# Optimization experiments

Measured on AMD Instinct MI355X. Metric: run time of the kernel, lower is better.

## Reference

```python
import jax, jax.numpy as jnp
import numpy as np

HYP_C = 0.1
TAU = 0.1
MRG = 0.1
CLIP_R = 2.3
BS = 1024
NB_PROXIES = 256
SZ_EMBED = 128
T_BATCH = BS * 50
T_LCA = NB_PROXIES * 50


@jax.custom_vjp
def artanh(x):
    xc = jnp.clip(x, -1.0 + 1e-5, 1.0 - 1e-5)
    return 0.5 * (jnp.log1p(xc) - jnp.log1p(-xc))

def _artanh_fwd(x):
    xc = jnp.clip(x, -1.0 + 1e-5, 1.0 - 1e-5)
    return 0.5 * (jnp.log1p(xc) - jnp.log1p(-xc)), xc

def _artanh_bwd(xc, g):
    return (g / (1.0 - xc * xc),)

artanh.defvjp(_artanh_fwd, _artanh_bwd)


@jax.custom_vjp
def riemannian_fix(x):
    # identity fwd; bwd rescales euclidean grad to riemannian grad on the ball
    return x

def _riem_fwd(x):
    return x, x

def _riem_bwd(x, g):
    scale = ((1.0 - HYP_C * jnp.sum(x * x, axis=-1, keepdims=True)) ** 2) / 4.0
    return (g * scale,)

riemannian_fix.defvjp(_riem_fwd, _riem_bwd)


def expmap0(x, c):
    sqrt_c = c ** 0.5
    xn = jnp.maximum(jnp.linalg.norm(x, axis=-1, keepdims=True), 1e-5)
    return jnp.tanh(sqrt_c * xn) * x / (sqrt_c * xn)


def project(x, c):
    norm = jnp.maximum(jnp.linalg.norm(x, axis=-1, keepdims=True), 1e-5)
    maxnorm = (1.0 - 1e-3) / (c ** 0.5)
    return jnp.where(norm > maxnorm, x / norm * maxnorm, x)


def to_poincare(x, c, clip_r):
    xn = jnp.linalg.norm(x, axis=-1, keepdims=True) + 1e-5
    x = x * jnp.minimum(jnp.ones_like(xn), clip_r / xn)
    return riemannian_fix(project(expmap0(x, c), c))


def dist_matrix(x, y, c):
    # ||mobius_add(-x, y)|| computed in closed form (same math as the [N,M,D]
    # num/denom construction in the torch code; num_{nm} = a*( -x_n ) + b*y_m).
    sqrt_c = c ** 0.5
    xy = -jnp.einsum('nd,md->nm', x, y)        # (-x) . y
    x2 = jnp.sum(x * x, axis=-1, keepdims=True)  # [N,1]
    y2t = jnp.sum(y * y, axis=-1)[None, :]       # [1,M]
    a = 1.0 + 2.0 * c * xy + c * y2t             # coeff of -x
    b = 1.0 - c * x2                             # coeff of y
    denom = 1.0 + 2.0 * c * xy + (c ** 2) * x2 * y2t
    num_sq = a * a * x2 + 2.0 * a * b * xy + b * b * y2t
    norm = jnp.sqrt(jnp.maximum(num_sq, 1e-12)) / jnp.abs(denom + 1e-5)
    return (2.0 / sqrt_c) * artanh(sqrt_c * norm)


def gumbel_softmax_hard(logits, g):
    # straight-through hard gumbel softmax (tau=1 as in F.gumbel_softmax default)
    y = jax.nn.softmax(logits + g, axis=-1)
    hard = jax.nn.one_hot(jnp.argmax(y, axis=-1), y.shape[-1], dtype=y.dtype)
    return y + jax.lax.stop_gradient(hard - y)


def compute_ghhc(cp_dist, trip, g):
    i, j, k = trip[0], trip[1], trip[2]
    di, dj, dk = cp_dist[i], cp_dist[j], cp_dist[k]   # [T,P] each
    max_ij = jnp.maximum(di, dj)
    p_ij = gumbel_softmax_hard(-max_ij / TAU, g[0])
    max_ijk = jnp.maximum(dk, max_ij)
    p_ijk = gumbel_softmax_hard(-max_ijk / TAU, g[1])
    diff_lca = (jnp.argmax(p_ij, -1) != jnp.argmax(p_ijk, -1)).astype(cp_dist.dtype)
    d_i_ij = jnp.sum(di * p_ij, axis=1)
    d_i_ijk = jnp.sum(di * p_ijk, axis=1)
    d_j_ij = jnp.sum(dj * p_ij, axis=1)
    d_j_ijk = jnp.sum(dj * p_ijk, axis=1)
    d_k_ij = jnp.sum(dk * p_ij, axis=1)
    d_k_ijk = jnp.sum(dk * p_ijk, axis=1)
    hc = (jax.nn.relu(d_i_ij - d_i_ijk + MRG)
          + jax.nn.relu(d_j_ij - d_j_ijk + MRG)
          + jax.nn.relu(d_k_ijk - d_k_ij + MRG))
    return jnp.mean(hc * diff_lca)


def hp_loss(z_s, t_s, lcas, trip1, trip2, trip3, trip4, g1, g2, g3, g4):
    bs = z_s.shape[0]
    lh = to_poincare(lcas, HYP_C, CLIP_R)
    all_nodes = jnp.concatenate([z_s, lh], axis=0)
    D = dist_matrix(all_nodes, all_nodes, HYP_C)
    t_all = jnp.concatenate([t_s, lh], axis=0)
    Dt = dist_matrix(t_all, t_all, HYP_C)
    loss = compute_ghhc(D[:bs, bs:], trip1, g1)
    loss = loss + compute_ghhc(D[bs:, bs:], trip2, g2)
    loss = loss + compute_ghhc(Dt[:bs, bs:], trip3, g3)
    loss = loss + compute_ghhc(Dt[bs:, bs:], trip4, g4)
    return loss


def setup_inputs() -> dict:
    key = jax.random.key(0)
    ks = jax.random.split(key, 12)
    z_s = jax.random.normal(ks[0], (BS, SZ_EMBED), dtype=jnp.float32)
    t_s = jax.random.normal(ks[1], (BS, SZ_EMBED), dtype=jnp.float32)
    y = jax.random.uniform(ks[2], (BS, 24), dtype=jnp.float32)
    # lcas param init: randn / sqrt(d) * clip_r * 0.9
    lcas = jax.random.normal(ks[3], (NB_PROXIES, SZ_EMBED), dtype=jnp.float32)
    lcas = lcas / np.sqrt(SZ_EMBED) * CLIP_R * 0.9
    trip1 = jax.random.randint(ks[4], (3, T_BATCH), 0, BS, dtype=jnp.int32)
    trip2 = jax.random.randint(ks[5], (3, T_LCA), 0, NB_PROXIES, dtype=jnp.int32)
    trip3 = jax.random.randint(ks[6], (3, T_BATCH), 0, BS, dtype=jnp.int32)
    trip4 = jax.random.randint(ks[7], (3, T_LCA), 0, NB_PROXIES, dtype=jnp.int32)
    g1 = jax.random.gumbel(ks[8], (2, T_BATCH, NB_PROXIES), dtype=jnp.float32)
    g2 = jax.random.gumbel(ks[9], (2, T_LCA, NB_PROXIES), dtype=jnp.float32)
    g3 = jax.random.gumbel(ks[10], (2, T_BATCH, NB_PROXIES), dtype=jnp.float32)
    g4 = jax.random.gumbel(ks[11], (2, T_LCA, NB_PROXIES), dtype=jnp.float32)
    return {"z_s": z_s, "t_s": t_s, "y": y, "lcas": lcas,
            "trip1": trip1, "trip2": trip2, "trip3": trip3, "trip4": trip4,
            "g1": g1, "g2": g2, "g3": g3, "g4": g4}


def reference(z_s, t_s, y, lcas, trip1, trip2, trip3, trip4, g1, g2, g3, g4):
    # y only feeds the detached numpy mining loop in the original; the mined
    # triplets are supplied precomputed (trip1..4), so y does not enter the math.
    return hp_loss(z_s, t_s, lcas, trip1, trip2, trip3, trip4, g1, g2, g3, g4)
```

## Files before the change

### kernel.cpp

```cpp
#include <hip/hip_runtime.h>
#include <cstddef>
#include <stdint.h>

#define HYP_C   0.1f
#define SQRT_C  0.31622776601683794f
#define CLIP_R  2.3f
#define MRG     0.1f
#define NPROX   256
#define DIM     128

#define OFF_LH   0
#define OFF_LHT  32768
#define OFF_LN2  65536
#define OFF_D1   65792
#define OFF_D2   327936
#define OFF_D3   393472

__global__ __launch_bounds__(128)
void to_poincare_kernel(const float* __restrict__ lcas,
                        float* __restrict__ ws,
                        float* __restrict__ out)
{
    const int row = blockIdx.x;
    const int k   = threadIdx.x;
    if (row == 0 && k == 0) out[0] = 0.0f;

    float v  = lcas[row * DIM + k];
    float ss = v * v;
    #pragma unroll
    for (int off = 32; off >= 1; off >>= 1)
        ss += __shfl_xor(ss, off, 64);
    __shared__ float wpart[2];
    if ((k & 63) == 0) wpart[k >> 6] = ss;
    __syncthreads();
    const float sumsq = wpart[0] + wpart[1];

    const float s1 = sqrtf(sumsq);
    const float xn = s1 + 1e-5f;
    const float f1 = fminf(1.0f, CLIP_R / xn);
    const float xn2 = fmaxf(f1 * s1, 1e-5f);
    const float th  = tanhf(SQRT_C * xn2);
    const float f2  = th / (SQRT_C * xn2);
    const float nr      = fmaxf(f2 * f1 * s1, 1e-5f);
    const float maxnorm = (1.0f - 1e-3f) / SQRT_C;
    const float f3      = (nr > maxnorm) ? (maxnorm / nr) : 1.0f;

    const float f  = f3 * f2 * f1;
    const float lv = f * v;
    ws[OFF_LH  + row * DIM + k]   = lv;
    ws[OFF_LHT + k * NPROX + row] = lv;
    if (k == 0) ws[OFF_LN2 + row] = f * f * sumsq;
}

__global__ __launch_bounds__(256)
void dist_all_kernel(const float* __restrict__ z,
                     const float* __restrict__ t,
                     float* __restrict__ ws, int nb1)
{
    const float* lhT = ws + OFF_LHT;
    const float* ln2 = ws + OFF_LN2;

    int b = blockIdx.x;
    const float* X; float* Dout; int row0;
    if (b < nb1)            { X = z;            Dout = ws + OFF_D1; row0 = b * 4; }
    else if (b < nb1 + 64)  { X = ws + OFF_LH;  Dout = ws + OFF_D2; row0 = (b - nb1) * 4; }
    else                    { X = t;            Dout = ws + OFF_D3; row0 = (b - nb1 - 64) * 4; }

    __shared__ float xs[4][DIM];
    __shared__ float sx2[4];

    for (int idx = threadIdx.x; idx < 4 * DIM; idx += 256)
        xs[idx / DIM][idx % DIM] = X[row0 * DIM + idx];
    __syncthreads();

    const int wid  = threadIdx.x >> 6;
    const int lane = threadIdx.x & 63;
    {
        float a = xs[wid][lane];
        float c = xs[wid][lane + 64];
        float s = a * a + c * c;
        #pragma unroll
        for (int off = 32; off >= 1; off >>= 1)
            s += __shfl_xor(s, off, 64);
        if (lane == 0) sx2[wid] = s;
    }
    __syncthreads();

    const int m = threadIdx.x;
    float dot0 = 0.f, dot1 = 0.f, dot2 = 0.f, dot3 = 0.f;
    #pragma unroll 8
    for (int k = 0; k < DIM; k += 4) {
        const float4 x0 = *(const float4*)&xs[0][k];
        const float4 x1 = *(const float4*)&xs[1][k];
        const float4 x2 = *(const float4*)&xs[2][k];
        const float4 x3 = *(const float4*)&xs[3][k];
        const float l0 = lhT[(k + 0) * NPROX + m];
        const float l1 = lhT[(k + 1) * NPROX + m];
        const float l2 = lhT[(k + 2) * NPROX + m];
        const float l3 = lhT[(k + 3) * NPROX + m];
        dot0 = fmaf(x0.x, l0, fmaf(x0.y, l1, fmaf(x0.z, l2, fmaf(x0.w, l3, dot0))));
        dot1 = fmaf(x1.x, l0, fmaf(x1.y, l1, fmaf(x1.z, l2, fmaf(x1.w, l3, dot1))));
        dot2 = fmaf(x2.x, l0, fmaf(x2.y, l1, fmaf(x2.z, l2, fmaf(x2.w, l3, dot2))));
        dot3 = fmaf(x3.x, l0, fmaf(x3.y, l1, fmaf(x3.z, l2, fmaf(x3.w, l3, dot3))));
    }

    const float y2 = ln2[m];
    float dots[4] = {dot0, dot1, dot2, dot3};
    #pragma unroll
    for (int r = 0; r < 4; ++r) {
        const float x2 = sx2[r];
        const float xy = -dots[r];
        const float a  = 1.0f + 2.0f * HYP_C * xy + HYP_C * y2;
        const float bb = 1.0f - HYP_C * x2;
        const float denom  = 1.0f + 2.0f * HYP_C * xy + HYP_C * HYP_C * x2 * y2;
        const float num_sq = a * a * x2 + 2.0f * a * bb * xy + bb * bb * y2;
        const float nrm = sqrtf(fmaxf(num_sq, 1e-12f)) / fabsf(denom + 1e-5f);
        float u = SQRT_C * nrm;
        u = fminf(fmaxf(u, -1.0f + 1e-5f), 1.0f - 1e-5f);
        const float d = (2.0f / SQRT_C) * (0.5f * (log1pf(u) - log1pf(-u)));
        Dout[(size_t)(row0 + r) * NPROX + m] = d;
    }
}

__device__ __forceinline__ float dpp_fmax16(float x) {
    int o;
    o = __builtin_amdgcn_update_dpp(0, __float_as_int(x), 0x121, 0xF, 0xF, true);
    x = fmaxf(x, __int_as_float(o));
    o = __builtin_amdgcn_update_dpp(0, __float_as_int(x), 0x122, 0xF, 0xF, true);
    x = fmaxf(x, __int_as_float(o));
    o = __builtin_amdgcn_update_dpp(0, __float_as_int(x), 0x124, 0xF, 0xF, true);
    x = fmaxf(x, __int_as_float(o));
    o = __builtin_amdgcn_update_dpp(0, __float_as_int(x), 0x128, 0xF, 0xF, true);
    x = fmaxf(x, __int_as_float(o));
    return x;
}

__device__ __forceinline__ int dpp_imax16(int x) {
    int o;
    o = __builtin_amdgcn_update_dpp(0, x, 0x121, 0xF, 0xF, true); x = max(x, o);
    o = __builtin_amdgcn_update_dpp(0, x, 0x122, 0xF, 0xF, true); x = max(x, o);
    o = __builtin_amdgcn_update_dpp(0, x, 0x124, 0xF, 0xF, true); x = max(x, o);
    o = __builtin_amdgcn_update_dpp(0, x, 0x128, 0xF, 0xF, true); x = max(x, o);
    return x;
}

__device__ __forceinline__ void amax4(float v0, float v1, float v2, float v3,
                                      int base, float& lv, int& li)
{
    if (v0 > lv) { lv = v0; li = base; }
    if (v1 > lv) { lv = v1; li = base + 1; }
    if (v2 > lv) { lv = v2; li = base + 2; }
    if (v3 > lv) { lv = v3; li = base + 3; }
}

__global__ __launch_bounds__(64, 4)
void ghhc_fused_kernel(const float* __restrict__ Da, const float* __restrict__ Db,
                       const float* __restrict__ Dc, const float* __restrict__ Dd,
                       const int* __restrict__ ta, const int* __restrict__ tb,
                       const int* __restrict__ tc, const int* __restrict__ td,
                       const float* __restrict__ ga, const float* __restrict__ gb,
                       const float* __restrict__ gc, const float* __restrict__ gd,
                       int Ta, int Tb, int Tc, int Td,
                       float sa, float sb, float sc_, float sd,
                       int nba, int nbb, int nbc,
                       float* __restrict__ out)
{
    const int lane = threadIdx.x;
    const int grp  = lane >> 4;
    const int hl   = lane & 15;

    const int b = blockIdx.x;
    const float* D; const int* tr; const float* g; int Tt; float sc; int lb;
    if (b < nba)                   { D = Da; tr = ta; g = ga; Tt = Ta; sc = sa;  lb = b; }
    else if (b < nba + nbb)        { D = Db; tr = tb; g = gb; Tt = Tb; sc = sb;  lb = b - nba; }
    else if (b < nba + nbb + nbc)  { D = Dc; tr = tc; g = gc; Tt = Tc; sc = sc_; lb = b - nba - nbb; }
    else                           { D = Dd; tr = td; g = gd; Tt = Td; sc = sd;  lb = b - nba - nbb - nbc; }

    const int tstart = lb * 32;
    float acc = 0.0f;

    #pragma unroll 2
    for (int it = 0; it < 8; ++it) {
        const int tt = tstart + it * 4 + grp;
        const bool ok = tt < Tt;
        const int ts = ok ? tt : (Tt - 1);
        const int i = tr[ts], j = tr[Tt + ts], kk = tr[2 * Tt + ts];

        const float4* Di = (const float4*)(D + (size_t)i  * NPROX);
        const float4* Dj = (const float4*)(D + (size_t)j  * NPROX);
        const float4* Dk = (const float4*)(D + (size_t)kk * NPROX);
        const float4* G0 = (const float4*)(g + (size_t)ts * NPROX);
        const float4* G1 = (const float4*)(g + ((size_t)Tt + ts) * NPROX);

        float lvA = -__builtin_inff(), lvB = -__builtin_inff();
        int   liA = 0, liB = 0;

        #pragma unroll
        for (int m = 0; m < 4; ++m) {
            const int q = m * 16 + hl;
            const float4 di = Di[q], dj = Dj[q], dk = Dk[q];
            const float4 g0 = G0[q], g1 = G1[q];

            const float m1x = fmaxf(di.x, dj.x), m1y = fmaxf(di.y, dj.y),
                        m1z = fmaxf(di.z, dj.z), m1w = fmaxf(di.w, dj.w);
            const float sx = fmaf(m1x, -10.0f, g0.x), sy = fmaf(m1y, -10.0f, g0.y),
                        sz = fmaf(m1z, -10.0f, g0.z), sw = fmaf(m1w, -10.0f, g0.w);
            const float m2x = fmaxf(dk.x, m1x), m2y = fmaxf(dk.y, m1y),
                        m2z = fmaxf(dk.z, m1z), m2w = fmaxf(dk.w, m1w);
            const float ux = fmaf(m2x, -10.0f, g1.x), uy = fmaf(m2y, -10.0f, g1.y),
                        uz = fmaf(m2z, -10.0f, g1.z), uw = fmaf(m2w, -10.0f, g1.w);

            const int base = m * 64 + hl * 4;
            amax4(sx, sy, sz, sw, base, lvA, liA);
            amax4(ux, uy, uz, uw, base, lvB, liB);
        }

        const float gvA = dpp_fmax16(lvA);
        const int   A   = 255 - dpp_imax16((lvA == gvA) ? (255 - liA) : 0);
        const float gvB = dpp_fmax16(lvB);
        const int   B   = 255 - dpp_imax16((lvB == gvB) ? (255 - liB) : 0);

        const float diA = D[(size_t)i  * NPROX + A], diB = D[(size_t)i  * NPROX + B];
        const float djA = D[(size_t)j  * NPROX + A], djB = D[(size_t)j  * NPROX + B];
        const float dkA = D[(size_t)kk * NPROX + A], dkB = D[(size_t)kk * NPROX + B];
        const float hc = fmaxf(diA - diB + MRG, 0.0f)
                       + fmaxf(djA - djB + MRG, 0.0f)
                       + fmaxf(dkB - dkA + MRG, 0.0f);
        acc += (ok && (A != B) && (hl == 0)) ? hc * sc : 0.0f;
    }

    #pragma unroll
    for (int off = 32; off >= 1; off >>= 1)
        acc += __shfl_xor(acc, off, 64);
    if (lane == 0)
        atomicAdd(out, acc);
}

extern "C" void kernel_launch(void* const* d_in, const int* in_sizes, int n_in,
                              void* d_out, int out_size, void* d_ws, size_t ws_size,
                              hipStream_t stream)
{
    const float* z_s  = (const float*)d_in[0];
    const float* t_s  = (const float*)d_in[1];
    const float* lcas = (const float*)d_in[3];
    const int* trip1 = (const int*)d_in[4];
    const int* trip2 = (const int*)d_in[5];
    const int* trip3 = (const int*)d_in[6];
    const int* trip4 = (const int*)d_in[7];
    const float* g1 = (const float*)d_in[8];
    const float* g2 = (const float*)d_in[9];
    const float* g3 = (const float*)d_in[10];
    const float* g4 = (const float*)d_in[11];
    float* out = (float*)d_out;
    float* ws  = (float*)d_ws;

    const int T1 = in_sizes[4] / 3;
    const int T2 = in_sizes[5] / 3;
    const int T3 = in_sizes[6] / 3;
    const int T4 = in_sizes[7] / 3;
    const int BS = in_sizes[0] / DIM;
    const int nb1 = BS / 4;

    to_poincare_kernel<<<NPROX, 128, 0, stream>>>(lcas, ws, out);

    dist_all_kernel<<<2 * nb1 + 64, 256, 0, stream>>>(z_s, t_s, ws, nb1);

    const int nbA = (T1 + 31) / 32;
    const int nbB = (T2 + 31) / 32;
    const int nbC = (T3 + 31) / 32;
    const int nbD = (T4 + 31) / 32;
    ghhc_fused_kernel<<<nbA + nbB + nbC + nbD, 64, 0, stream>>>(
        ws + OFF_D1, ws + OFF_D2, ws + OFF_D3, ws + OFF_D2,
        trip1, trip2, trip3, trip4,
        g1, g2, g3, g4,
        T1, T2, T3, T4,
        1.0f / (float)T1, 1.0f / (float)T2, 1.0f / (float)T3, 1.0f / (float)T4,
        nbA, nbB, nbC,
        out);
}
```

Baseline: 350.9 us.

## Restructure triplet argmax kernel: register-held rows, DPP value broadcast, 256-thread blocks

Each wave now handles 16 triplets per block, and blocks grow from 64 to 256 threads. Triplet indices are prefetched up front. The D and Gumbel rows are held in registers, so the argmax winner's distances are broadcast with DPP max reductions instead of being re-gathered with six scattered global loads. Argmax tie-breaking now keeps the lowest index through a separate pass plus a DPP min. The cross-wave sum goes through shared memory, so there are fewer atomics. The aim is to cut dependent global gathers and per-block overhead, at the cost of more register pressure and less per-wave triplet work.

```diff
diff --git a/kernel.cpp b/kernel.cpp
--- a/kernel.cpp
+++ b/kernel.cpp
@@ -135,25 +135,16 @@
     return x;
 }
 
-__device__ __forceinline__ int dpp_imax16(int x) {
+__device__ __forceinline__ int dpp_imin16(int x) {
     int o;
-    o = __builtin_amdgcn_update_dpp(0, x, 0x121, 0xF, 0xF, true); x = max(x, o);
-    o = __builtin_amdgcn_update_dpp(0, x, 0x122, 0xF, 0xF, true); x = max(x, o);
-    o = __builtin_amdgcn_update_dpp(0, x, 0x124, 0xF, 0xF, true); x = max(x, o);
-    o = __builtin_amdgcn_update_dpp(0, x, 0x128, 0xF, 0xF, true); x = max(x, o);
+    o = __builtin_amdgcn_update_dpp(0, x, 0x121, 0xF, 0xF, true); x = min(x, o);
+    o = __builtin_amdgcn_update_dpp(0, x, 0x122, 0xF, 0xF, true); x = min(x, o);
+    o = __builtin_amdgcn_update_dpp(0, x, 0x124, 0xF, 0xF, true); x = min(x, o);
+    o = __builtin_amdgcn_update_dpp(0, x, 0x128, 0xF, 0xF, true); x = min(x, o);
     return x;
 }
 
-__device__ __forceinline__ void amax4(float v0, float v1, float v2, float v3,
-                                      int base, float& lv, int& li)
-{
-    if (v0 > lv) { lv = v0; li = base; }
-    if (v1 > lv) { lv = v1; li = base + 1; }
-    if (v2 > lv) { lv = v2; li = base + 2; }
-    if (v3 > lv) { lv = v3; li = base + 3; }
-}
-
-__global__ __launch_bounds__(64, 4)
+__global__ __launch_bounds__(256)
 void ghhc_fused_kernel(const float* __restrict__ Da, const float* __restrict__ Db,
                        const float* __restrict__ Dc, const float* __restrict__ Dd,
                        const int* __restrict__ ta, const int* __restrict__ tb,
@@ -165,9 +156,11 @@
                        int nba, int nbb, int nbc,
                        float* __restrict__ out)
 {
-    const int lane = threadIdx.x;
-    const int grp  = lane >> 4;
-    const int hl   = lane & 15;
+    const int tid = threadIdx.x;
+    const int w   = tid >> 6;
+    const int grp = (tid >> 4) & 3;
+    const int hl  = tid & 15;
+    const int hl4 = hl << 2;
 
     const int b = blockIdx.x;
     const float* D; const int* tr; const float* g; int Tt; float sc; int lb;
@@ -176,64 +169,98 @@
     else if (b < nba + nbb + nbc)  { D = Dc; tr = tc; g = gc; Tt = Tc; sc = sc_; lb = b - nba - nbb; }
     else                           { D = Dd; tr = td; g = gd; Tt = Td; sc = sd;  lb = b - nba - nbb - nbc; }
 
-    const int tstart = lb * 32;
+    const int tstart = lb * 64 + w * 16;
+
+    int iIt[4], jIt[4], kIt[4]; bool okIt[4];
+    #pragma unroll
+    for (int it = 0; it < 4; ++it) {
+        int t = tstart + it * 4 + grp;
+        okIt[it] = (t < Tt);
+        t = okIt[it] ? t : (Tt - 1);
+        iIt[it] = tr[t]; jIt[it] = tr[Tt + t]; kIt[it] = tr[2 * Tt + t];
+    }
+
     float acc = 0.0f;
 
-    #pragma unroll 2
-    for (int it = 0; it < 8; ++it) {
-        const int tt = tstart + it * 4 + grp;
-        const bool ok = tt < Tt;
-        const int ts = ok ? tt : (Tt - 1);
-        const int i = tr[ts], j = tr[Tt + ts], kk = tr[2 * Tt + ts];
+    #pragma unroll 1
+    for (int it = 0; it < 4; ++it) {
+        int t = tstart + it * 4 + grp;
+        t = okIt[it] ? t : (Tt - 1);
+        const int i = iIt[it], j = jIt[it], kk = kIt[it];
 
         const float4* Di = (const float4*)(D + (size_t)i  * NPROX);
         const float4* Dj = (const float4*)(D + (size_t)j  * NPROX);
         const float4* Dk = (const float4*)(D + (size_t)kk * NPROX);
-        const float4* G0 = (const float4*)(g + (size_t)ts * NPROX);
-        const float4* G1 = (const float4*)(g + ((size_t)Tt + ts) * NPROX);
-
-        float lvA = -__builtin_inff(), lvB = -__builtin_inff();
-        int   liA = 0, liB = 0;
-
+        const float4* G0 = (const float4*)(g + (size_t)t * NPROX);
+        const float4* G1 = (const float4*)(g + ((size_t)Tt + t) * NPROX);
+
+        float dif[16], djf[16], dkf[16], g0f[16], g1f[16];
         #pragma unroll
         for (int m = 0; m < 4; ++m) {
             const int q = m * 16 + hl;
-            const float4 di = Di[q], dj = Dj[q], dk = Dk[q];
-            const float4 g0 = G0[q], g1 = G1[q];
-
-            const float m1x = fmaxf(di.x, dj.x), m1y = fmaxf(di.y, dj.y),
-                        m1z = fmaxf(di.z, dj.z), m1w = fmaxf(di.w, dj.w);
-            const float sx = fmaf(m1x, -10.0f, g0.x), sy = fmaf(m1y, -10.0f, g0.y),
-                        sz = fmaf(m1z, -10.0f, g0.z), sw = fmaf(m1w, -10.0f, g0.w);
-            const float m2x = fmaxf(dk.x, m1x), m2y = fmaxf(dk.y, m1y),
-                        m2z = fmaxf(dk.z, m1z), m2w = fmaxf(dk.w, m1w);
-            const float ux = fmaf(m2x, -10.0f, g1.x), uy = fmaf(m2y, -10.0f, g1.y),
-                        uz = fmaf(m2z, -10.0f, g1.z), uw = fmaf(m2w, -10.0f, g1.w);
-
-            const int base = m * 64 + hl * 4;
-            amax4(sx, sy, sz, sw, base, lvA, liA);
-            amax4(ux, uy, uz, uw, base, lvB, liB);
+            float4 v;
+            v = Di[q]; dif[m*4+0]=v.x; dif[m*4+1]=v.y; dif[m*4+2]=v.z; dif[m*4+3]=v.w;
+            v = Dj[q]; djf[m*4+0]=v.x; djf[m*4+1]=v.y; djf[m*4+2]=v.z; djf[m*4+3]=v.w;
+            v = Dk[q]; dkf[m*4+0]=v.x; dkf[m*4+1]=v.y; dkf[m*4+2]=v.z; dkf[m*4+3]=v.w;
+            v = G0[q]; g0f[m*4+0]=v.x; g0f[m*4+1]=v.y; g0f[m*4+2]=v.z; g0f[m*4+3]=v.w;
+            v = G1[q]; g1f[m*4+0]=v.x; g1f[m*4+1]=v.y; g1f[m*4+2]=v.z; g1f[m*4+3]=v.w;
         }
 
+        float Sf[16], Uf[16];
+        #pragma unroll
+        for (int c = 0; c < 16; ++c) {
+            const float m1 = fmaxf(dif[c], djf[c]);
+            Sf[c] = fmaf(m1, -10.0f, g0f[c]);
+            const float m2 = fmaxf(dkf[c], m1);
+            Uf[c] = fmaf(m2, -10.0f, g1f[c]);
+        }
+
+        float lvA = Sf[0], lvB = Uf[0];
+        #pragma unroll
+        for (int c = 1; c < 16; ++c) { lvA = fmaxf(lvA, Sf[c]); lvB = fmaxf(lvB, Uf[c]); }
         const float gvA = dpp_fmax16(lvA);
-        const int   A   = 255 - dpp_imax16((lvA == gvA) ? (255 - liA) : 0);
         const float gvB = dpp_fmax16(lvB);
-        const int   B   = 255 - dpp_imax16((lvB == gvB) ? (255 - liB) : 0);
-
-        const float diA = D[(size_t)i  * NPROX + A], diB = D[(size_t)i  * NPROX + B];
-        const float djA = D[(size_t)j  * NPROX + A], djB = D[(size_t)j  * NPROX + B];
-        const float dkA = D[(size_t)kk * NPROX + A], dkB = D[(size_t)kk * NPROX + B];
+
+        int slA = 64, slB = 64;
+        float pAi = -1.f, pAj = -1.f, pAk = -1.f;
+        float pBi = -1.f, pBj = -1.f, pBk = -1.f;
+        #pragma unroll
+        for (int c = 15; c >= 0; --c) {
+            const bool mA = (Sf[c] == gvA);
+            slA = mA ? c : slA;
+            pAi = mA ? dif[c] : pAi; pAj = mA ? djf[c] : pAj; pAk = mA ? dkf[c] : pAk;
+            const bool mB = (Uf[c] == gvB);
+            slB = mB ? c : slB;
+            pBi = mB ? dif[c] : pBi; pBj = mB ? djf[c] : pBj; pBk = mB ? dkf[c] : pBk;
+        }
+
+        const int eA = (slA < 16) ? (((slA & 12) << 4) | (hl4 | (slA & 3))) : 1024;
+        const int eB = (slB < 16) ? (((slB & 12) << 4) | (hl4 | (slB & 3))) : 1024;
+        const int Ag = dpp_imin16(eA);
+        const int Bg = dpp_imin16(eB);
+
+        const bool ownA = (eA == Ag);
+        const bool ownB = (eB == Bg);
+        const float diA = dpp_fmax16(ownA ? pAi : -1.f);
+        const float djA = dpp_fmax16(ownA ? pAj : -1.f);
+        const float dkA = dpp_fmax16(ownA ? pAk : -1.f);
+        const float diB = dpp_fmax16(ownB ? pBi : -1.f);
+        const float djB = dpp_fmax16(ownB ? pBj : -1.f);
+        const float dkB = dpp_fmax16(ownB ? pBk : -1.f);
+
         const float hc = fmaxf(diA - diB + MRG, 0.0f)
                        + fmaxf(djA - djB + MRG, 0.0f)
                        + fmaxf(dkB - dkA + MRG, 0.0f);
-        acc += (ok && (A != B) && (hl == 0)) ? hc * sc : 0.0f;
-    }
-
-    #pragma unroll
-    for (int off = 32; off >= 1; off >>= 1)
-        acc += __shfl_xor(acc, off, 64);
-    if (lane == 0)
-        atomicAdd(out, acc);
+        acc += (okIt[it] && (Ag != Bg) && (hl == 0)) ? hc * sc : 0.0f;
+    }
+
+    acc += __shfl_xor(acc, 16, 64);
+    acc += __shfl_xor(acc, 32, 64);
+    __shared__ float wsum[4];
+    if ((tid & 63) == 0) wsum[w] = acc;
+    __syncthreads();
+    if (tid == 0)
+        atomicAdd(out, wsum[0] + wsum[1] + wsum[2] + wsum[3]);
 }
 
 extern "C" void kernel_launch(void* const* d_in, const int* in_sizes, int n_in,
@@ -265,11 +292,11 @@
 
     dist_all_kernel<<<2 * nb1 + 64, 256, 0, stream>>>(z_s, t_s, ws, nb1);
 
-    const int nbA = (T1 + 31) / 32;
-    const int nbB = (T2 + 31) / 32;
-    const int nbC = (T3 + 31) / 32;
-    const int nbD = (T4 + 31) / 32;
-    ghhc_fused_kernel<<<nbA + nbB + nbC + nbD, 64, 0, stream>>>(
+    const int nbA = (T1 + 63) / 64;
+    const int nbB = (T2 + 63) / 64;
+    const int nbC = (T3 + 63) / 64;
+    const int nbD = (T4 + 63) / 64;
+    ghhc_fused_kernel<<<nbA + nbB + nbC + nbD, 256, 0, stream>>>(
         ws + OFF_D1, ws + OFF_D2, ws + OFF_D3, ws + OFF_D2,
         trip1, trip2, trip3, trip4,
         g1, g2, g3, g4,
```

Measured after the change: 300.9 us. 1.17x faster.
